# Kernel tuning notes

Measured on AMD Instinct MI355X. Metric: run time of the kernel, lower is better.

The kernel has to match this reference:

```python
import jax, jax.numpy as jnp
import numpy as np

NEG_SLOPE = 0.2  # PyG GATConv default negative_slope


def setup_inputs() -> dict:
    key = jax.random.key(0)
    ks = jax.random.split(key, 10)
    B, N, E = 8, 10000, 160000
    Din, Dout = 128, 128
    x = jax.random.normal(ks[0], (B, N, Din), dtype=jnp.float32)
    src = jax.random.randint(ks[1], (E,), 0, N)
    dst = jax.random.randint(ks[2], (E,), 0, N)
    edge_index = jnp.stack([src, dst])  # [2, E]
    edge_attr = jax.random.uniform(ks[3], (E,), dtype=jnp.float32)
    lim = 1.0 / np.sqrt(Din)
    W = jax.random.uniform(ks[4], (Dout, Din), jnp.float32, -lim, lim)   # shared lin (src==dst)
    We = jax.random.uniform(ks[5], (Dout, 1), jnp.float32, -1.0, 1.0)    # lin_edge, edge_dim=1
    att_src = jax.random.normal(ks[6], (Dout,), jnp.float32) * 0.1
    att_dst = jax.random.normal(ks[7], (Dout,), jnp.float32) * 0.1
    att_edge = jax.random.normal(ks[8], (Dout,), jnp.float32) * 0.1
    bias = jnp.zeros((Dout,), jnp.float32)
    return {"x": x, "edge_index": edge_index, "edge_attr": edge_attr,
            "W": W, "We": We, "att_src": att_src, "att_dst": att_dst,
            "att_edge": att_edge, "bias": bias}


def reference(x, edge_index, edge_attr, W, We, att_src, att_dst, att_edge, bias):
    B, N, Din = x.shape
    src, dst = edge_index[0], edge_index[1]
    # --- add self loops with fill_value='mean' (mean of incoming edge_attr per node) ---
    deg = jax.ops.segment_sum(jnp.ones_like(edge_attr), dst, num_segments=N)
    loop_attr = jax.ops.segment_sum(edge_attr, dst, num_segments=N) / jnp.maximum(deg, 1.0)
    ar = jnp.arange(N, dtype=src.dtype)
    full_src = jnp.concatenate([src, ar])          # [E2]
    full_dst = jnp.concatenate([dst, ar])          # [E2]
    full_attr = jnp.concatenate([edge_attr, loop_attr])
    # edge features: Linear(1 -> Dout, no bias) == outer product; identical across batch
    e_feat = full_attr[:, None] * We[:, 0][None, :]        # [E2, Dout]
    alpha_e = e_feat @ att_edge                            # [E2]

    def single(xb):  # xb: [N, Din]
        h = xb @ W.T                                       # [N, Dout]
        a_src = h @ att_src                                # [N]
        a_dst = h @ att_dst                                # [N]
        a = a_src[full_src] + a_dst[full_dst] + alpha_e    # [E2]
        a = jax.nn.leaky_relu(a, NEG_SLOPE)
        # segment softmax over destination node
        a_max = jax.ops.segment_max(a, full_dst, num_segments=N)
        a_max = jnp.where(jnp.isfinite(a_max), a_max, 0.0)
        ex = jnp.exp(a - a_max[full_dst])
        s = jax.ops.segment_sum(ex, full_dst, num_segments=N)
        alpha = ex / (s[full_dst] + 1e-16)                 # [E2]
        out = jax.ops.segment_sum(alpha[:, None] * h[full_src], full_dst, num_segments=N)
        return out + bias, alpha

    x_out, attn = jax.vmap(single)(x)   # [B, N, Dout], [B, E2]
    return x_out, attn
```

## Files before the change

### kernel.cpp

```cpp
#include <hip/hip_runtime.h>
#include <hip/hip_bf16.h>
#include <hip/hip_fp16.h>

typedef short short8 __attribute__((ext_vector_type(8)));
typedef float floatx4 __attribute__((ext_vector_type(4)));

static constexpr int BATCH = 8;
static constexpr int NN    = 10000;
static constexpr int EE    = 160000;
static constexpr int EE2   = EE + NN;
static constexpr int DD    = 128;
static constexpr int STR   = 64;
static constexpr float SLOPE = 0.2f;
static constexpr long OUT_ELEMS = (long)BATCH * NN * DD;
static constexpr int EB = EE / 256;

__device__ inline float ldf(const void* p, long i, int f32) {
    return f32 ? ((const float*)p)[i]
               : __bfloat162float(((const __hip_bfloat16*)p)[i]);
}
__device__ inline int esrc(const int* ei, int e, int i64) { return i64 ? ei[2 * e] : ei[e]; }
__device__ inline int edst(const int* ei, int e, int i64) { return i64 ? ei[2 * (EE + e)] : ei[EE + e]; }
__device__ inline short bf16bits(float v) {
    __hip_bfloat16 b = __float2bfloat16(v);
    short s; __builtin_memcpy(&s, &b, 2); return s;
}
__device__ inline short f16bits(float v) {
    __half b = __float2half(v);
    short s; __builtin_memcpy(&s, &b, 2); return s;
}

__global__ __launch_bounds__(256) void k_detect(const unsigned short* __restrict__ xu,
                                                const int* __restrict__ ei,
                                                const void* __restrict__ We,
                                                const void* __restrict__ att_edge,
                                                int* __restrict__ flags,
                                                float* __restrict__ cout,
                                                int* __restrict__ deg) {
    int t = threadIdx.x;
    if (blockIdx.x > 0) {
        int idx = (blockIdx.x - 1) * 256 + t;
        if (idx < NN) deg[idx] = 0;
        return;
    }
    __shared__ int cnt[2];
    __shared__ float red[256];
    if (t < 2) cnt[t] = 0;
    __syncthreads();
    int c1 = 0;
    for (int i = t; i < 32768; i += 256) {
        unsigned short u = xu[i];
        if ((u & 0x7F80u) == 0x7F80u) c1++;
    }
    int c2 = (ei[2 * t + 1] != 0) ? 1 : 0;
    if (c1) atomicAdd(&cnt[0], c1);
    if (c2) atomicAdd(&cnt[1], c2);
    __syncthreads();
    int f32 = (cnt[0] > 0);
    if (t == 0) { flags[0] = f32; flags[1] = (cnt[1] == 0); }
    red[t] = (t < DD) ? ldf(We, t, f32) * ldf(att_edge, t, f32) : 0.f;
    __syncthreads();
    for (int o = 128; o > 0; o >>= 1) {
        if (t < o) red[t] += red[t + o];
        __syncthreads();
    }
    if (t == 0) *cout = red[0];
}

__global__ __launch_bounds__(256) void k_bucket(const int* __restrict__ ei,
                                                const void* __restrict__ attr,
                                                const void* __restrict__ W,
                                                const int* __restrict__ flags,
                                                int* __restrict__ deg,
                                                int2* __restrict__ edgesP,
                                                __hip_bfloat16* __restrict__ Wb) {
    int f32 = flags[0], i64 = flags[1];
    int bId = blockIdx.x, t = threadIdx.x;
    if (bId < EB) {
        int e = bId * 256 + t;
        int d = edst(ei, e, i64);
        int s = esrc(ei, e, i64);
        float at = ldf(attr, e, f32);
        int p = atomicAdd(&deg[d], 1);
        if (p < STR) edgesP[d * STR + p] = make_int2(s, __float_as_int(at));
    } else {
        int idx = (bId - EB) * 512 + t * 2;
        if (f32) {
            float2 v = ((const float2*)W)[idx >> 1];
            Wb[idx]     = __float2bfloat16(v.x);
            Wb[idx + 1] = __float2bfloat16(v.y);
        } else {
            ((ushort2*)Wb)[idx >> 1] = ((const ushort2*)W)[idx >> 1];
        }
    }
}

template<int F32>
__device__ inline void load_a(const void* __restrict__ x, long row, int quad, short8 afr[4]) {
    if (F32) {
        const float* xr = (const float*)x + row * DD;
        #pragma unroll
        for (int kk = 0; kk < 4; kk++) {
            float4 f0 = *(const float4*)(xr + kk * 32 + quad * 8);
            float4 f1 = *(const float4*)(xr + kk * 32 + quad * 8 + 4);
            short8 a;
            a[0] = bf16bits(f0.x); a[1] = bf16bits(f0.y); a[2] = bf16bits(f0.z); a[3] = bf16bits(f0.w);
            a[4] = bf16bits(f1.x); a[5] = bf16bits(f1.y); a[6] = bf16bits(f1.z); a[7] = bf16bits(f1.w);
            afr[kk] = a;
        }
    } else {
        const short* xr = (const short*)x + row * DD;
        #pragma unroll
        for (int kk = 0; kk < 4; kk++)
            afr[kk] = *(const short8*)(xr + kk * 32 + quad * 8);
    }
}

__global__ __launch_bounds__(128) void k_gemm(const void* __restrict__ x,
                                              const __hip_bfloat16* __restrict__ Wb,
                                              const void* __restrict__ att_src,
                                              const void* __restrict__ att_dst,
                                              const int* __restrict__ flags,
                                              short* __restrict__ h,
                                              float* __restrict__ asrc_t, float* __restrict__ adst_t) {
    __shared__ float tile[2][16 * 132];
    int f32 = flags[0];
    int wave = threadIdx.x >> 6;
    int lane = threadIdx.x & 63;
    int l15  = lane & 15, quad = lane >> 4;
    long rows_base = (long)blockIdx.x * 32 + wave * 16;

    short8 afr[4];
    if (f32) load_a<1>(x, rows_base + l15, quad, afr);
    else     load_a<0>(x, rows_base + l15, quad, afr);

    const short* wr = (const short*)Wb;
    floatx4 acc[8];
    #pragma unroll
    for (int jt = 0; jt < 8; jt++) acc[jt] = (floatx4){0.f, 0.f, 0.f, 0.f};
    #pragma unroll
    for (int jt = 0; jt < 8; jt++) {
        #pragma unroll
        for (int kk = 0; kk < 4; kk++) {
            short8 bfr = *(const short8*)(wr + (jt * 16 + l15) * DD + kk * 32 + quad * 8);
            acc[jt] = __builtin_amdgcn_mfma_f32_16x16x32_bf16(afr[kk], bfr, acc[jt], 0, 0, 0);
        }
    }

    float asum[4] = {0.f, 0.f, 0.f, 0.f};
    float dsum[4] = {0.f, 0.f, 0.f, 0.f};
    #pragma unroll
    for (int jt = 0; jt < 8; jt++) {
        int col = jt * 16 + l15;
        float as = ldf(att_src, col, f32);
        float ad = ldf(att_dst, col, f32);
        #pragma unroll
        for (int r = 0; r < 4; r++) {
            asum[r] += acc[jt][r] * as;
            dsum[r] += acc[jt][r] * ad;
        }
    }
    #pragma unroll
    for (int r = 0; r < 4; r++) {
        float a = asum[r], d = dsum[r];
        #pragma unroll
        for (int o = 1; o < 16; o <<= 1) { a += __shfl_xor(a, o, 64); d += __shfl_xor(d, o, 64); }
        if (l15 == 0) {
            long row = rows_base + quad * 4 + r;
            int b = (int)(row / NN), n = (int)(row - (long)b * NN);
            asrc_t[n * 8 + b] = a;
            adst_t[n * 8 + b] = d;
        }
    }

    float* tl = &tile[wave][0];
    #pragma unroll
    for (int jt = 0; jt < 8; jt++)
        #pragma unroll
        for (int r = 0; r < 4; r++)
            tl[(quad * 4 + r) * 132 + jt * 16 + l15] = acc[jt][r];
    #pragma unroll
    for (int it = 0; it < 4; it++) {
        int row = it * 4 + quad;
        float4 f0 = *(const float4*)&tl[row * 132 + l15 * 8];
        float4 f1 = *(const float4*)&tl[row * 132 + l15 * 8 + 4];
        short8 o;
        o[0] = f16bits(f0.x); o[1] = f16bits(f0.y); o[2] = f16bits(f0.z); o[3] = f16bits(f0.w);
        o[4] = f16bits(f1.x); o[5] = f16bits(f1.y); o[6] = f16bits(f1.z); o[7] = f16bits(f1.w);
        *(short8*)(h + (rows_base + row) * DD + l15 * 8) = o;
    }
}

__global__ __launch_bounds__(256, 4) void k_agg(const int2* __restrict__ edgesP,
                                                const float* __restrict__ asrc_t,
                                                const float* __restrict__ adst_t,
                                                const __half* __restrict__ h,
                                                const int* __restrict__ deg,
                                                const float* __restrict__ cptr,
                                                const void* __restrict__ bias,
                                                const int* __restrict__ flags,
                                                float* __restrict__ invT,
                                                float* __restrict__ latc,
                                                void* __restrict__ outbuf) {
    int f32 = flags[0];
    int tid = threadIdx.x;
    int lane = tid & 63;
    int g   = lane >> 4;
    int c16 = tid & 15;
    int wv  = tid >> 6;
    int laneBase = lane & 48;
    int b = blockIdx.x & 7;
    int n = (blockIdx.x >> 3) * 16 + wv * 4 + g;

    float c   = *cptr;
    int dg    = min(deg[n], STR);
    int np    = (dg + 1) >> 1;
    float an  = adst_t[n * 8 + b];

    const int2* em = edgesP + (long)n * STR;
    const __half* hb = h + (long)b * NN * DD;

    float acc[8];
    #pragma unroll
    for (int j = 0; j < 8; j++) acc[j] = 0.f;
    float ssum = 0.f, sattr = 0.f;

#define LOADM(K, DST)                                                       \
    {   int _idx = (K) * 16 + c16;                                          \
        if (_idx < dg) DST = em[_idx];                                      \
        else { DST.x = n; DST.y = 0; }                                      \
    }

#define MSTEP(PD)                                                           \
    if (((PD) & 7) == 0) {                                                  \
        int _kc = ((PD) >> 3) + 1;                                          \
        int2 _t; LOADM(_kc, _t);                                            \
        if (_kc & 1) mvB = _t; else mvA = _t;                               \
    }

#define DISSUE(PD, HV0, HV1, AR0, AR1, AT0, AT1)                            \
    {   int _j0 = ((PD) << 1) & 15;                                         \
        int _mx = (((PD) >> 3) & 1) ? mvB.x : mvA.x;                        \
        int _my = (((PD) >> 3) & 1) ? mvB.y : mvA.y;                        \
        int _s0 = __shfl(_mx, laneBase | _j0);                              \
        int _s1 = __shfl(_mx, laneBase | (_j0 + 1));                        \
        AT0 = __int_as_float(__shfl(_my, laneBase | _j0));                  \
        AT1 = __int_as_float(__shfl(_my, laneBase | (_j0 + 1)));            \
        AR0 = asrc_t[_s0 * 8 + b];                                          \
        AR1 = asrc_t[_s1 * 8 + b];                                          \
        HV0 = *(const uint4*)(hb + (long)_s0 * DD + c16 * 8);               \
        HV1 = *(const uint4*)(hb + (long)_s1 * DD + c16 * 8);               \
    }

#define CONSUME(P, HV0, HV1, AR0, AR1, AT0, AT1)                            \
    {   sattr += AT0;                                                       \
        float _a0 = fmaf(c, AT0, AR0 + an);                                 \
        _a0 = fmaxf(_a0, SLOPE * _a0);                                      \
        float _e0 = __expf(_a0);                                            \
        ssum += _e0;                                                        \
        const __half* _h0 = (const __half*)&HV0;                            \
        _Pragma("unroll")                                                   \
        for (int _j = 0; _j < 8; _j++)                                      \
            acc[_j] += _e0 * __half2float(_h0[_j]);                         \
        if (2 * (P) + 1 < dg) {                                             \
            sattr += AT1;                                                   \
            float _a1 = fmaf(c, AT1, AR1 + an);                             \
            _a1 = fmaxf(_a1, SLOPE * _a1);                                  \
            float _e1 = __expf(_a1);                                        \
            ssum += _e1;                                                    \
            const __half* _h1 = (const __half*)&HV1;                        \
            _Pragma("unroll")                                               \
            for (int _j = 0; _j < 8; _j++)                                  \
                acc[_j] += _e1 * __half2float(_h1[_j]);                     \
        }                                                                   \
    }

    int2 mvA, mvB;
    LOADM(0, mvA);
    LOADM(1, mvB);
    uint4 z4 = {0, 0, 0, 0};
    uint4 hA0 = z4, hA1 = z4, hB0 = z4, hB1 = z4, hC0 = z4, hC1 = z4,
          hD0 = z4, hD1 = z4, hE0 = z4, hE1 = z4;
    float arA0 = 0.f, arA1 = 0.f, atA0 = 0.f, atA1 = 0.f;
    float arB0 = 0.f, arB1 = 0.f, atB0 = 0.f, atB1 = 0.f;
    float arC0 = 0.f, arC1 = 0.f, atC0 = 0.f, atC1 = 0.f;
    float arD0 = 0.f, arD1 = 0.f, atD0 = 0.f, atD1 = 0.f;
    float arE0 = 0.f, arE1 = 0.f, atE0 = 0.f, atE1 = 0.f;
    if (0 < np) DISSUE(0, hA0, hA1, arA0, arA1, atA0, atA1);
    if (1 < np) DISSUE(1, hB0, hB1, arB0, arB1, atB0, atB1);
    if (2 < np) DISSUE(2, hC0, hC1, arC0, arC1, atC0, atC1);
    if (3 < np) DISSUE(3, hD0, hD1, arD0, arD1, atD0, atD1);

    for (int p = 0; p < np; p += 5) {
        MSTEP(p + 4);
        if (p + 4 < np) DISSUE(p + 4, hE0, hE1, arE0, arE1, atE0, atE1);
        CONSUME(p, hA0, hA1, arA0, arA1, atA0, atA1);
        if (p + 1 >= np) break;
        MSTEP(p + 5);
        if (p + 5 < np) DISSUE(p + 5, hA0, hA1, arA0, arA1, atA0, atA1);
        CONSUME(p + 1, hB0, hB1, arB0, arB1, atB0, atB1);
        if (p + 2 >= np) break;
        MSTEP(p + 6);
        if (p + 6 < np) DISSUE(p + 6, hB0, hB1, arB0, arB1, atB0, atB1);
        CONSUME(p + 2, hC0, hC1, arC0, arC1, atC0, atC1);
        if (p + 3 >= np) break;
        MSTEP(p + 7);
        if (p + 7 < np) DISSUE(p + 7, hC0, hC1, arC0, arC1, atC0, atC1);
        CONSUME(p + 3, hD0, hD1, arD0, arD1, atD0, atD1);
        if (p + 4 >= np) break;
        MSTEP(p + 8);
        if (p + 8 < np) DISSUE(p + 8, hD0, hD1, arD0, arD1, atD0, atD1);
        CONSUME(p + 4, hE0, hE1, arE0, arE1, atE0, atE1);
    }
#undef LOADM
#undef MSTEP
#undef DISSUE
#undef CONSUME

    float mean = sattr / fmaxf((float)dg, 1.0f);
    {
        float ars = asrc_t[n * 8 + b];
        float a = fmaf(c, mean, ars + an);
        a = fmaxf(a, SLOPE * a);
        float ex = __expf(a);
        ssum += ex;
        uint4 hv = *(const uint4*)(hb + (long)n * DD + c16 * 8);
        const __half* hh = (const __half*)&hv;
        #pragma unroll
        for (int j = 0; j < 8; j++) acc[j] += ex * __half2float(hh[j]);
    }
    if (c16 == 0 && b == 0) latc[n] = mean;

    float inv = 1.0f / (ssum + 1e-16f);
    if (c16 == 0) invT[n * 8 + b] = inv;
    #pragma unroll
    for (int j = 0; j < 8; j++) acc[j] = acc[j] * inv + ldf(bias, c16 * 8 + j, f32);

    long row = (long)b * NN + n;
    if (f32) {
        float4 lo = {acc[0], acc[1], acc[2], acc[3]};
        float4 hi = {acc[4], acc[5], acc[6], acc[7]};
        float4* orow = (float4*)((float*)outbuf + row * DD);
        orow[c16 * 2]     = lo;
        orow[c16 * 2 + 1] = hi;
    } else {
        short8 o;
        #pragma unroll
        for (int j = 0; j < 8; j++) o[j] = bf16bits(acc[j]);
        ((short8*)((__hip_bfloat16*)outbuf + row * DD))[c16] = o;
    }
}

__global__ __launch_bounds__(256) void k_attn(const int* __restrict__ ei,
                                              const void* __restrict__ attr,
                                              const float* __restrict__ asrc_t,
                                              const float* __restrict__ adst_t,
                                              const float* __restrict__ latc,
                                              const float* __restrict__ cptr,
                                              const float* __restrict__ invT,
                                              const int* __restrict__ flags,
                                              void* __restrict__ outbuf) {
    int f32 = flags[0], i64 = flags[1];
    int e2 = blockIdx.x * 256 + threadIdx.x;
    if (e2 >= EE2) return;
    float c = *cptr;
    int s, d; float at;
    if (e2 < EE) {
        s = esrc(ei, e2, i64);
        d = edst(ei, e2, i64);
        at = ldf(attr, e2, f32);
    } else {
        int nn = e2 - EE;
        s = nn; d = nn;
        at = latc[nn];
    }
    float4 as0 = *(const float4*)(asrc_t + (long)s * 8);
    float4 as1 = *(const float4*)(asrc_t + (long)s * 8 + 4);
    float4 ad0 = *(const float4*)(adst_t + (long)d * 8);
    float4 ad1 = *(const float4*)(adst_t + (long)d * 8 + 4);
    float4 iv0 = *(const float4*)(invT   + (long)d * 8);
    float4 iv1 = *(const float4*)(invT   + (long)d * 8 + 4);
    float asv[8] = {as0.x, as0.y, as0.z, as0.w, as1.x, as1.y, as1.z, as1.w};
    float adv[8] = {ad0.x, ad0.y, ad0.z, ad0.w, ad1.x, ad1.y, ad1.z, ad1.w};
    float ivv[8] = {iv0.x, iv0.y, iv0.z, iv0.w, iv1.x, iv1.y, iv1.z, iv1.w};
    float ca = c * at;
    #pragma unroll
    for (int b = 0; b < BATCH; b++) {
        float a = asv[b] + adv[b] + ca;
        a = (a > 0.f) ? a : SLOPE * a;
        float al = __expf(a) * ivv[b];
        long gidx = OUT_ELEMS + (long)b * EE2 + e2;
        if (f32) ((float*)outbuf)[gidx] = al;
        else     ((__hip_bfloat16*)outbuf)[gidx] = __float2bfloat16(al);
    }
}

extern "C" void kernel_launch(void* const* d_in, const int* in_sizes, int n_in,
                              void* d_out, int out_size, void* d_ws, size_t ws_size,
                              hipStream_t stream) {
    const void* x        = d_in[0];
    const int*  ei       = (const int*)d_in[1];
    const void* attr     = d_in[2];
    const void* W        = d_in[3];
    const void* We       = d_in[4];
    const void* att_src  = d_in[5];
    const void* att_dst  = d_in[6];
    const void* att_edge = d_in[7];
    const void* bias     = d_in[8];

    char* ws = (char*)d_ws;
    size_t off = 0;
    auto alloc = [&](size_t bytes) { size_t o = off; off = (off + bytes + 255) & ~(size_t)255; return o; };
    short* h             = (short*)(ws + alloc((size_t)BATCH * NN * DD * 2));
    float* asrc_t        = (float*)(ws + alloc((size_t)NN * 8 * 4));
    float* adst_t        = (float*)(ws + alloc((size_t)NN * 8 * 4));
    float* invT          = (float*)(ws + alloc((size_t)NN * 8 * 4));
    int*   deg           = (int*)  (ws + alloc((size_t)NN * 4));
    float* latc          = (float*)(ws + alloc((size_t)NN * 4));
    int2*  edgesP        = (int2*) (ws + alloc((size_t)NN * STR * 8));
    __hip_bfloat16* Wb   = (__hip_bfloat16*)(ws + alloc((size_t)DD * DD * 2));
    float* cscal         = (float*)(ws + alloc(256));
    int*   flags         = (int*)  (ws + alloc(256));

    k_detect<<<41, 256, 0, stream>>>((const unsigned short*)x, ei, We, att_edge,
                                     flags, cscal, deg);
    k_bucket<<<EB + 32, 256, 0, stream>>>(ei, attr, W, flags, deg, edgesP, Wb);
    k_gemm  <<<(BATCH * NN) / 32, 128, 0, stream>>>(x, Wb, att_src, att_dst, flags,
                                                    h, asrc_t, adst_t);
    k_agg   <<<(BATCH * NN) / 16, 256, 0, stream>>>(edgesP, asrc_t, adst_t, (const __half*)h,
                                                    deg, cscal, bias, flags,
                                                    invT, latc, d_out);
    k_attn  <<<(EE2 + 255) / 256, 256, 0, stream>>>(ei, attr, asrc_t, adst_t, latc,
                                                    cscal, invT, flags, d_out);
}
```

Before: 221.1 us.

## Precompute edge weights cooperatively into LDS and pipeline gathers from shared metadata

Each 16-lane group now loads its node's 64-entry edge list as int4 pairs, computes the attention logits and exponentials for all edges in parallel, and stores (weight, src) pairs into shared memory. The aggregation loop then reads the metadata from LDS and runs a deeper, 3-4 stage prefetch of h rows, doing only FMAs in the inner loop, with ssum and sattr reduced across lanes afterwards. This removes the per-edge shuffles and redundant exp/asrc loads done by all 16 lanes. The trade-off is extra LDS traffic, and the loop now runs to the wave-wide maximum degree, so padded slots (self index, zero weight) still issue h loads.

```diff
diff --git a/kernel.cpp b/kernel.cpp
--- a/kernel.cpp
+++ b/kernel.cpp
@@ -202,125 +202,102 @@
                                                 float* __restrict__ invT,
                                                 float* __restrict__ latc,
                                                 void* __restrict__ outbuf) {
+    __shared__ float4 smeta[16 * 36 + 16];
     int f32 = flags[0];
     int tid = threadIdx.x;
     int lane = tid & 63;
     int g   = lane >> 4;
     int c16 = tid & 15;
     int wv  = tid >> 6;
-    int laneBase = lane & 48;
     int b = blockIdx.x & 7;
     int n = (blockIdx.x >> 3) * 16 + wv * 4 + g;
 
-    float c   = *cptr;
+    float cc  = *cptr;
     int dg    = min(deg[n], STR);
-    int np    = (dg + 1) >> 1;
     float an  = adst_t[n * 8 + b];
 
-    const int2* em = edgesP + (long)n * STR;
     const __half* hb = h + (long)b * NN * DD;
+    float4* qptr = smeta + (wv * 4 + g) * 36;
+
+    const int4* em4 = (const int4*)(edgesP + (long)n * STR);
+    int4 mr0 = em4[c16];
+    int4 mr1 = em4[16 + c16];
 
     float acc[8];
     #pragma unroll
     for (int j = 0; j < 8; j++) acc[j] = 0.f;
     float ssum = 0.f, sattr = 0.f;
 
-#define LOADM(K, DST)                                                       \
-    {   int _idx = (K) * 16 + c16;                                          \
-        if (_idx < dg) DST = em[_idx];                                      \
-        else { DST.x = n; DST.y = 0; }                                      \
-    }
-
-#define MSTEP(PD)                                                           \
-    if (((PD) & 7) == 0) {                                                  \
-        int _kc = ((PD) >> 3) + 1;                                          \
-        int2 _t; LOADM(_kc, _t);                                            \
-        if (_kc & 1) mvB = _t; else mvA = _t;                               \
-    }
-
-#define DISSUE(PD, HV0, HV1, AR0, AR1, AT0, AT1)                            \
-    {   int _j0 = ((PD) << 1) & 15;                                         \
-        int _mx = (((PD) >> 3) & 1) ? mvB.x : mvA.x;                        \
-        int _my = (((PD) >> 3) & 1) ? mvB.y : mvA.y;                        \
-        int _s0 = __shfl(_mx, laneBase | _j0);                              \
-        int _s1 = __shfl(_mx, laneBase | (_j0 + 1));                        \
-        AT0 = __int_as_float(__shfl(_my, laneBase | _j0));                  \
-        AT1 = __int_as_float(__shfl(_my, laneBase | (_j0 + 1)));            \
-        AR0 = asrc_t[_s0 * 8 + b];                                          \
-        AR1 = asrc_t[_s1 * 8 + b];                                          \
-        HV0 = *(const uint4*)(hb + (long)_s0 * DD + c16 * 8);               \
-        HV1 = *(const uint4*)(hb + (long)_s1 * DD + c16 * 8);               \
-    }
-
-#define CONSUME(P, HV0, HV1, AR0, AR1, AT0, AT1)                            \
-    {   sattr += AT0;                                                       \
-        float _a0 = fmaf(c, AT0, AR0 + an);                                 \
-        _a0 = fmaxf(_a0, SLOPE * _a0);                                      \
-        float _e0 = __expf(_a0);                                            \
-        ssum += _e0;                                                        \
-        const __half* _h0 = (const __half*)&HV0;                            \
-        _Pragma("unroll")                                                   \
-        for (int _j = 0; _j < 8; _j++)                                      \
-            acc[_j] += _e0 * __half2float(_h0[_j]);                         \
-        if (2 * (P) + 1 < dg) {                                             \
-            sattr += AT1;                                                   \
-            float _a1 = fmaf(c, AT1, AR1 + an);                             \
-            _a1 = fmaxf(_a1, SLOPE * _a1);                                  \
-            float _e1 = __expf(_a1);                                        \
-            ssum += _e1;                                                    \
-            const __half* _h1 = (const __half*)&HV1;                        \
-            _Pragma("unroll")                                               \
-            for (int _j = 0; _j < 8; _j++)                                  \
-                acc[_j] += _e1 * __half2float(_h1[_j]);                     \
-        }                                                                   \
-    }
-
-    int2 mvA, mvB;
-    LOADM(0, mvA);
-    LOADM(1, mvB);
-    uint4 z4 = {0, 0, 0, 0};
-    uint4 hA0 = z4, hA1 = z4, hB0 = z4, hB1 = z4, hC0 = z4, hC1 = z4,
-          hD0 = z4, hD1 = z4, hE0 = z4, hE1 = z4;
-    float arA0 = 0.f, arA1 = 0.f, atA0 = 0.f, atA1 = 0.f;
-    float arB0 = 0.f, arB1 = 0.f, atB0 = 0.f, atB1 = 0.f;
-    float arC0 = 0.f, arC1 = 0.f, atC0 = 0.f, atC1 = 0.f;
-    float arD0 = 0.f, arD1 = 0.f, atD0 = 0.f, atD1 = 0.f;
-    float arE0 = 0.f, arE1 = 0.f, atE0 = 0.f, atE1 = 0.f;
-    if (0 < np) DISSUE(0, hA0, hA1, arA0, arA1, atA0, atA1);
-    if (1 < np) DISSUE(1, hB0, hB1, arB0, arB1, atB0, atB1);
-    if (2 < np) DISSUE(2, hC0, hC1, arC0, arC1, atC0, atC1);
-    if (3 < np) DISSUE(3, hD0, hD1, arD0, arD1, atD0, atD1);
-
-    for (int p = 0; p < np; p += 5) {
-        MSTEP(p + 4);
-        if (p + 4 < np) DISSUE(p + 4, hE0, hE1, arE0, arE1, atE0, atE1);
-        CONSUME(p, hA0, hA1, arA0, arA1, atA0, atA1);
-        if (p + 1 >= np) break;
-        MSTEP(p + 5);
-        if (p + 5 < np) DISSUE(p + 5, hA0, hA1, arA0, arA1, atA0, atA1);
-        CONSUME(p + 1, hB0, hB1, arB0, arB1, atB0, atB1);
-        if (p + 2 >= np) break;
-        MSTEP(p + 6);
-        if (p + 6 < np) DISSUE(p + 6, hB0, hB1, arB0, arB1, atB0, atB1);
-        CONSUME(p + 2, hC0, hC1, arC0, arC1, atC0, atC1);
-        if (p + 3 >= np) break;
-        MSTEP(p + 7);
-        if (p + 7 < np) DISSUE(p + 7, hC0, hC1, arC0, arC1, atC0, atC1);
-        CONSUME(p + 3, hD0, hD1, arD0, arD1, atD0, atD1);
-        if (p + 4 >= np) break;
-        MSTEP(p + 8);
-        if (p + 8 < np) DISSUE(p + 8, hD0, hD1, arD0, arD1, atD0, atD1);
-        CONSUME(p + 4, hE0, hE1, arE0, arE1, atE0, atE1);
-    }
-#undef LOADM
-#undef MSTEP
-#undef DISSUE
-#undef CONSUME
+#define STAGE(CH, MR)                                                        \
+    {   int _e0 = (CH) * 32 + 2 * c16;                                       \
+        bool _v0 = _e0 < dg, _v1 = (_e0 + 1) < dg;                           \
+        int _s0 = _v0 ? MR.x : n;                                            \
+        int _s1 = _v1 ? MR.z : n;                                            \
+        float _at0 = _v0 ? __int_as_float(MR.y) : 0.f;                       \
+        float _at1 = _v1 ? __int_as_float(MR.w) : 0.f;                       \
+        float _ar0 = asrc_t[_s0 * 8 + b];                                    \
+        float _ar1 = asrc_t[_s1 * 8 + b];                                    \
+        float _a0 = fmaf(cc, _at0, _ar0 + an); _a0 = fmaxf(_a0, SLOPE * _a0);\
+        float _a1 = fmaf(cc, _at1, _ar1 + an); _a1 = fmaxf(_a1, SLOPE * _a1);\
+        float _ex0 = _v0 ? __expf(_a0) : 0.f;                                \
+        float _ex1 = _v1 ? __expf(_a1) : 0.f;                                \
+        ssum += _ex0 + _ex1; sattr += _at0 + _at1;                           \
+        qptr[(CH) * 16 + c16] = make_float4(_ex0, __int_as_float(_s0),       \
+                                            _ex1, __int_as_float(_s1));      \
+    }
+
+    STAGE(0, mr0);
+    STAGE(1, mr1);
+
+    int npq = (dg + 1) >> 1;
+    int t1  = max(npq, __shfl_xor(npq, 16, 64));
+    int npw = max(t1, __shfl_xor(t1, 32, 64));
+
+#define DSR(S, MD)   MD = qptr[(S)];
+#define HISS(MH, V0, V1)                                                     \
+    {   int _s0 = __float_as_int(MH.y), _s1 = __float_as_int(MH.w);          \
+        V0 = *(const uint4*)(hb + (long)_s0 * DD + c16 * 8);                 \
+        V1 = *(const uint4*)(hb + (long)_s1 * DD + c16 * 8); }
+#define FMA8(MF, V0, V1)                                                     \
+    {   float _e0 = MF.x, _e1 = MF.z;                                        \
+        const __half* _p0 = (const __half*)&V0;                              \
+        const __half* _p1 = (const __half*)&V1;                              \
+        _Pragma("unroll")                                                    \
+        for (int _j = 0; _j < 8; _j++) acc[_j] += _e0 * __half2float(_p0[_j]);\
+        _Pragma("unroll")                                                    \
+        for (int _j = 0; _j < 8; _j++) acc[_j] += _e1 * __half2float(_p1[_j]);\
+    }
+
+    float4 m0, m1, m2, m3, m4, m5, m6, m7;
+    uint4 hA0, hA1, hB0, hB1, hC0, hC1, hD0, hD1;
+    DSR(0, m0); DSR(1, m1); DSR(2, m2); DSR(3, m3); DSR(4, m4); DSR(5, m5);
+    HISS(m0, hA0, hA1); HISS(m1, hB0, hB1); HISS(m2, hC0, hC1);
+
+    for (int p = 0; p < npw; p += 8) {
+        DSR(p + 6,  m6); HISS(m3, hD0, hD1); FMA8(m0, hA0, hA1);
+        if (p + 1 < npw) { DSR(p + 7,  m7); HISS(m4, hA0, hA1); FMA8(m1, hB0, hB1); }
+        if (p + 2 < npw) { DSR(p + 8,  m0); HISS(m5, hB0, hB1); FMA8(m2, hC0, hC1); }
+        if (p + 3 < npw) { DSR(p + 9,  m1); HISS(m6, hC0, hC1); FMA8(m3, hD0, hD1); }
+        if (p + 4 < npw) { DSR(p + 10, m2); HISS(m7, hD0, hD1); FMA8(m4, hA0, hA1); }
+        if (p + 5 < npw) { DSR(p + 11, m3); HISS(m0, hA0, hA1); FMA8(m5, hB0, hB1); }
+        if (p + 6 < npw) { DSR(p + 12, m4); HISS(m1, hB0, hB1); FMA8(m6, hC0, hC1); }
+        if (p + 7 < npw) { DSR(p + 13, m5); HISS(m2, hC0, hC1); FMA8(m7, hD0, hD1); }
+    }
+#undef STAGE
+#undef DSR
+#undef HISS
+#undef FMA8
+
+    #pragma unroll
+    for (int o = 1; o < 16; o <<= 1) {
+        ssum  += __shfl_xor(ssum, o, 64);
+        sattr += __shfl_xor(sattr, o, 64);
+    }
 
     float mean = sattr / fmaxf((float)dg, 1.0f);
     {
         float ars = asrc_t[n * 8 + b];
-        float a = fmaf(c, mean, ars + an);
+        float a = fmaf(cc, mean, ars + an);
         a = fmaxf(a, SLOPE * a);
         float ex = __expf(a);
         ssum += ex;
```

After: 223.2 us. Within noise of the previous version (+0.9%).
